# Kernel tuning notes

Hardware: AMD Instinct MI355X
Metric: run time of the kernel (lower is better)

## Reference

```python
import jax, jax.numpy as jnp
import numpy as np

NUM_EXPERTS = 8
IN_FEATURES = 2048
OUT_FEATURES = 5632
GROUP_SIZE = 64
NUM_TOKENS = 4096


def setup_inputs() -> dict:
    key = jax.random.key(0)
    k1, k2, k3, k4 = jax.random.split(key, 4)
    inp = jax.random.normal(k1, (NUM_TOKENS, IN_FEATURES), dtype=jnp.float32)
    # tokens are pre-sorted contiguously per expert; balanced routing
    tokens_per_expert = jnp.full((NUM_EXPERTS,), NUM_TOKENS // NUM_EXPERTS, dtype=jnp.int32)
    # int4 quantized weights stored as integer codes in [0, 16)
    weights = jax.random.randint(k2, (NUM_EXPERTS, IN_FEATURES, OUT_FEATURES), 0, 16, dtype=jnp.int32)
    n_groups = IN_FEATURES // GROUP_SIZE
    scales = jax.random.uniform(k3, (NUM_EXPERTS, n_groups, OUT_FEATURES, 1), dtype=jnp.float32,
                                minval=0.005, maxval=0.02)
    zeros = jax.random.normal(k4, (NUM_EXPERTS, n_groups, OUT_FEATURES, 1), dtype=jnp.float32) * 0.01
    scales_and_zeros = jnp.concatenate([scales, zeros], axis=-1)  # [E, K//G, N, 2]
    return {"input": inp, "tokens_per_expert": tokens_per_expert,
            "weights": weights, "scales_and_zeros": scales_and_zeros}


def _dequant(weights, scales_and_zeros):
    # torchao int4 convention: w = (q - 8) * scale + zero, grouped along K
    E, K, N = weights.shape
    n_groups = scales_and_zeros.shape[1]
    g = K // n_groups
    q = weights.astype(jnp.float32).reshape(E, n_groups, g, N)
    s = scales_and_zeros[..., 0][:, :, None, :]  # [E, K//G, 1, N]
    z = scales_and_zeros[..., 1][:, :, None, :]
    return ((q - 8.0) * s + z).reshape(E, K, N)


def reference(input, tokens_per_expert, weights, scales_and_zeros):
    num_tokens, K = input.shape
    E = weights.shape[0]
    W = _dequant(weights, scales_and_zeros)  # [E, K, N] float32
    # expert id of each (contiguous-sorted) token from cumsum boundaries
    cum = jnp.cumsum(tokens_per_expert)                      # [E]
    seg = jnp.searchsorted(cum, jnp.arange(num_tokens), side='right')  # [T]
    start = jnp.concatenate([jnp.zeros((1,), cum.dtype), cum[:-1]])
    pos = jnp.arange(num_tokens) - start[seg]                # slot within expert block
    # capacity-based grouped GEMM (balanced routing in setup: C = T // E)
    C = num_tokens // E
    buf = jnp.zeros((E, C, K), input.dtype).at[seg, pos].set(input)
    y = jnp.einsum('eck,ekn->ecn', buf, W)                   # per-expert GEMM
    return y[seg, pos]                                       # [T, N]
```

## Files before the change

### kernel.cpp

```cpp
#include <hip/hip_runtime.h>

#define NE    8
#define KDIM  2048
#define NDIM  5632
#define NTOK  4096
#define CAP   512
#define NGRP  32
#define BM    128
#define BN    128
#define BK    32
#define MT    4
#define NT    44
#define LDSS  40

typedef __attribute__((ext_vector_type(8))) short bf16x8;
typedef __attribute__((ext_vector_type(4))) short bf16x4;
typedef __attribute__((ext_vector_type(4))) float f32x4;

static __device__ __forceinline__ short f2bf(float f) {
    union { float f; unsigned u; } x; x.f = f;
    unsigned r = (x.u + 0x7fffu + ((x.u >> 16) & 1u)) >> 16;
    return (short)r;
}

__global__ __launch_bounds__(256, 2)
void hqq_gemm_kernel(const float* __restrict__ inp,
                     const int*   __restrict__ wq,
                     const float* __restrict__ sz,
                     float*       __restrict__ out)
{
    const int bid = blockIdx.x;
    const int e   = bid / (MT * NT);
    const int rem = bid % (MT * NT);
    const int nt  = rem >> 2;
    const int mt  = rem & 3;

    __shared__ __align__(16) short Alds[BM * LDSS];
    __shared__ __align__(16) short Blds[BN * LDSS];

    const int tid = threadIdx.x;
    const int m0  = e * CAP + mt * BM;
    const int n0  = nt * BN;

    const int a_kq  = tid & 7;
    const int a_row = tid >> 3;
    const int b_n   = tid & 127;
    const int b_h   = tid >> 7;

    const float* Ab  = inp + (size_t)m0 * KDIM;
    const int*   Wb  = wq  + (size_t)e * KDIM * NDIM + n0 + b_n;
    const float* SZb = sz  + (size_t)e * NGRP * (NDIM * 2) + (size_t)(n0 + b_n) * 2;

    f32x4 acc[4][4];
    #pragma unroll
    for (int i = 0; i < 4; ++i)
        #pragma unroll
        for (int j = 0; j < 4; ++j)
            acc[i][j] = (f32x4){0.f, 0.f, 0.f, 0.f};

    const int wave = tid >> 6;
    const int lane = tid & 63;
    const int wm = (wave >> 1) << 6;
    const int wn = (wave & 1) << 6;
    const int lr = lane & 15;
    const int lq = lane >> 4;

    for (int k0 = 0; k0 < KDIM; k0 += BK) {
        const int g = k0 >> 6;

        #pragma unroll
        for (int p = 0; p < 4; ++p) {
            const int row = a_row + p * 32;
            const float4 v = *(const float4*)(Ab + (size_t)row * KDIM + k0 + a_kq * 4);
            bf16x4 h;
            h[0] = f2bf(v.x); h[1] = f2bf(v.y); h[2] = f2bf(v.z); h[3] = f2bf(v.w);
            *(bf16x4*)&Alds[row * LDSS + a_kq * 4] = h;
        }

        const float2 s2 = *(const float2*)(SZb + (size_t)g * (NDIM * 2));
        const float s  = s2.x;
        const float z8 = s2.y - 8.f * s2.x;
        #pragma unroll
        for (int oo = 0; oo < 2; ++oo) {
            const int ko = b_h * 8 + oo * 16;
            const int* wp = Wb + (size_t)(k0 + ko) * NDIM;
            bf16x8 bb;
            #pragma unroll
            for (int j = 0; j < 8; ++j) {
                const float q = (float)wp[(size_t)j * NDIM];
                bb[j] = f2bf(fmaf(q, s, z8));
            }
            *(bf16x8*)&Blds[b_n * LDSS + ko] = bb;
        }

        __syncthreads();

        bf16x8 af[4], bfv[4];
        #pragma unroll
        for (int i = 0; i < 4; ++i)
            af[i] = *(const bf16x8*)&Alds[(wm + i * 16 + lr) * LDSS + lq * 8];
        #pragma unroll
        for (int j = 0; j < 4; ++j)
            bfv[j] = *(const bf16x8*)&Blds[(wn + j * 16 + lr) * LDSS + lq * 8];
        #pragma unroll
        for (int i = 0; i < 4; ++i)
            #pragma unroll
            for (int j = 0; j < 4; ++j)
                acc[i][j] = __builtin_amdgcn_mfma_f32_16x16x32_bf16(af[i], bfv[j], acc[i][j], 0, 0, 0);

        __syncthreads();
    }

    const int orow0 = m0 + wm + lq * 4;
    const int ocol0 = n0 + wn + lr;
    #pragma unroll
    for (int i = 0; i < 4; ++i)
        #pragma unroll
        for (int r = 0; r < 4; ++r) {
            float* op = out + (size_t)(orow0 + i * 16 + r) * NDIM + ocol0;
            #pragma unroll
            for (int j = 0; j < 4; ++j)
                op[j * 16] = acc[i][j][r];
        }
}

extern "C" void kernel_launch(void* const* d_in, const int* in_sizes, int n_in,
                              void* d_out, int out_size, void* d_ws, size_t ws_size,
                              hipStream_t stream) {
    const float* inp = (const float*)d_in[0];
    const int*   wq  = (const int*)d_in[2];
    const float* sz  = (const float*)d_in[3];
    float*       out = (float*)d_out;

    dim3 grid(NE * MT * NT);
    hqq_gemm_kernel<<<grid, dim3(256), 0, stream>>>(inp, wq, sz, out);
}
```

Baseline: 683.5 us.

## Prepack int4 weights into nibbles and pre-convert activations to bf16

A new pre-pass kernel packs the int32 weight codes into 4-bit nibbles (eight per word) and converts the fp32 input to bf16 in workspace memory. The GEMM then reads the packed weights and bf16 activations, which reduces the bytes the four M-tiles pull per expert and drops the per-tile conversions. The pre-pass still reads all int32 weights once and adds a launch. The original kernel is kept as a fallback when the workspace is too small.

```diff
diff --git a/kernel.cpp b/kernel.cpp
--- a/kernel.cpp
+++ b/kernel.cpp
@@ -13,6 +13,13 @@
 #define NT    44
 #define LDSS  40
 
+#define K8      (KDIM / 8)
+#define NBLK_N  (NDIM / 256)
+#define PACK_BLOCKS (NE * K8 * NBLK_N)
+#define ACV_BLOCKS  (NTOK * KDIM / (8 * 256))
+#define PACKED_BYTES ((size_t)NE * K8 * NDIM * 4)
+#define ABF_BYTES    ((size_t)NTOK * KDIM * 2)
+
 typedef __attribute__((ext_vector_type(8))) short bf16x8;
 typedef __attribute__((ext_vector_type(4))) short bf16x4;
 typedef __attribute__((ext_vector_type(4))) float f32x4;
@@ -23,11 +30,39 @@
     return (short)r;
 }
 
+__global__ __launch_bounds__(256)
+void pack_kernel(const int* __restrict__ wq, const float* __restrict__ inp,
+                 unsigned* __restrict__ pw, unsigned short* __restrict__ abf)
+{
+    const int bid = blockIdx.x;
+    if (bid < PACK_BLOCKS) {
+        const int e  = bid / (K8 * NBLK_N);
+        const int r  = bid % (K8 * NBLK_N);
+        const int k8 = r / NBLK_N;
+        const int nb = r % NBLK_N;
+        const int n  = nb * 256 + threadIdx.x;
+        const int* src = wq + ((size_t)e * KDIM + k8 * 8) * NDIM + n;
+        unsigned v = 0;
+        #pragma unroll
+        for (int j = 0; j < 8; ++j)
+            v |= (unsigned)(src[(size_t)j * NDIM] & 15) << (4 * j);
+        pw[((size_t)e * K8 + k8) * NDIM + n] = v;
+    } else {
+        const size_t t = (size_t)(bid - PACK_BLOCKS) * 256 + threadIdx.x;
+        const float4* p = (const float4*)inp + t * 2;
+        const float4 v0 = p[0], v1 = p[1];
+        bf16x8 h;
+        h[0] = f2bf(v0.x); h[1] = f2bf(v0.y); h[2] = f2bf(v0.z); h[3] = f2bf(v0.w);
+        h[4] = f2bf(v1.x); h[5] = f2bf(v1.y); h[6] = f2bf(v1.z); h[7] = f2bf(v1.w);
+        *((bf16x8*)abf + t) = h;
+    }
+}
+
 __global__ __launch_bounds__(256, 2)
-void hqq_gemm_kernel(const float* __restrict__ inp,
-                     const int*   __restrict__ wq,
-                     const float* __restrict__ sz,
-                     float*       __restrict__ out)
+void hqq_gemm2(const unsigned short* __restrict__ abf,
+               const unsigned*       __restrict__ pw,
+               const float*          __restrict__ sz,
+               float*                __restrict__ out)
 {
     const int bid = blockIdx.x;
     const int e   = bid / (MT * NT);
@@ -42,14 +77,14 @@
     const int m0  = e * CAP + mt * BM;
     const int n0  = nt * BN;
 
-    const int a_kq  = tid & 7;
-    const int a_row = tid >> 3;
+    const int a_kq  = tid & 3;
+    const int a_row = tid >> 2;
     const int b_n   = tid & 127;
     const int b_h   = tid >> 7;
 
-    const float* Ab  = inp + (size_t)m0 * KDIM;
-    const int*   Wb  = wq  + (size_t)e * KDIM * NDIM + n0 + b_n;
-    const float* SZb = sz  + (size_t)e * NGRP * (NDIM * 2) + (size_t)(n0 + b_n) * 2;
+    const unsigned short* Ab = abf + (size_t)m0 * KDIM;
+    const unsigned*       Wb = pw  + (size_t)e * K8 * NDIM + n0 + b_n;
+    const float*          SZb = sz + (size_t)e * NGRP * (NDIM * 2) + (size_t)(n0 + b_n) * 2;
 
     f32x4 acc[4][4];
     #pragma unroll
@@ -69,6 +104,103 @@
         const int g = k0 >> 6;
 
         #pragma unroll
+        for (int p = 0; p < 2; ++p) {
+            const int row = a_row + p * 64;
+            const bf16x8 v = *(const bf16x8*)(Ab + (size_t)row * KDIM + k0 + a_kq * 8);
+            *(bf16x8*)&Alds[row * LDSS + a_kq * 8] = v;
+        }
+
+        const float2 s2 = *(const float2*)(SZb + (size_t)g * (NDIM * 2));
+        const float s  = s2.x;
+        const float z8 = s2.y - 8.f * s2.x;
+        const unsigned* wp = Wb + ((size_t)(k0 >> 3) + b_h * 2) * NDIM;
+        const unsigned u0 = wp[0];
+        const unsigned u1 = wp[NDIM];
+        bf16x8 bb0, bb1;
+        #pragma unroll
+        for (int j = 0; j < 8; ++j) {
+            bb0[j] = f2bf(fmaf((float)((u0 >> (4 * j)) & 15u), s, z8));
+            bb1[j] = f2bf(fmaf((float)((u1 >> (4 * j)) & 15u), s, z8));
+        }
+        *(bf16x8*)&Blds[b_n * LDSS + b_h * 16]     = bb0;
+        *(bf16x8*)&Blds[b_n * LDSS + b_h * 16 + 8] = bb1;
+
+        __syncthreads();
+
+        bf16x8 af[4], bfv[4];
+        #pragma unroll
+        for (int i = 0; i < 4; ++i)
+            af[i] = *(const bf16x8*)&Alds[(wm + i * 16 + lr) * LDSS + lq * 8];
+        #pragma unroll
+        for (int j = 0; j < 4; ++j)
+            bfv[j] = *(const bf16x8*)&Blds[(wn + j * 16 + lr) * LDSS + lq * 8];
+        #pragma unroll
+        for (int i = 0; i < 4; ++i)
+            #pragma unroll
+            for (int j = 0; j < 4; ++j)
+                acc[i][j] = __builtin_amdgcn_mfma_f32_16x16x32_bf16(af[i], bfv[j], acc[i][j], 0, 0, 0);
+
+        __syncthreads();
+    }
+
+    const int orow0 = m0 + wm + lq * 4;
+    const int ocol0 = n0 + wn + lr;
+    #pragma unroll
+    for (int i = 0; i < 4; ++i)
+        #pragma unroll
+        for (int r = 0; r < 4; ++r) {
+            float* op = out + (size_t)(orow0 + i * 16 + r) * NDIM + ocol0;
+            #pragma unroll
+            for (int j = 0; j < 4; ++j)
+                op[j * 16] = acc[i][j][r];
+        }
+}
+
+__global__ __launch_bounds__(256, 2)
+void hqq_gemm_fallback(const float* __restrict__ inp,
+                       const int*   __restrict__ wq,
+                       const float* __restrict__ sz,
+                       float*       __restrict__ out)
+{
+    const int bid = blockIdx.x;
+    const int e   = bid / (MT * NT);
+    const int rem = bid % (MT * NT);
+    const int nt  = rem >> 2;
+    const int mt  = rem & 3;
+
+    __shared__ __align__(16) short Alds[BM * LDSS];
+    __shared__ __align__(16) short Blds[BN * LDSS];
+
+    const int tid = threadIdx.x;
+    const int m0  = e * CAP + mt * BM;
+    const int n0  = nt * BN;
+
+    const int a_kq  = tid & 7;
+    const int a_row = tid >> 3;
+    const int b_n   = tid & 127;
+    const int b_h   = tid >> 7;
+
+    const float* Ab  = inp + (size_t)m0 * KDIM;
+    const int*   Wb  = wq  + (size_t)e * KDIM * NDIM + n0 + b_n;
+    const float* SZb = sz  + (size_t)e * NGRP * (NDIM * 2) + (size_t)(n0 + b_n) * 2;
+
+    f32x4 acc[4][4];
+    #pragma unroll
+    for (int i = 0; i < 4; ++i)
+        #pragma unroll
+        for (int j = 0; j < 4; ++j)
+            acc[i][j] = (f32x4){0.f, 0.f, 0.f, 0.f};
+
+    const int wave = tid >> 6;
+    const int lane = tid & 63;
+    const int wm = (wave >> 1) << 6;
+    const int wn = (wave & 1) << 6;
+    const int lr = lane & 15;
+    const int lq = lane >> 4;
+
+    for (int k0 = 0; k0 < KDIM; k0 += BK) {
+        const int g = k0 >> 6;
+        #pragma unroll
         for (int p = 0; p < 4; ++p) {
             const int row = a_row + p * 32;
             const float4 v = *(const float4*)(Ab + (size_t)row * KDIM + k0 + a_kq * 4);
@@ -76,7 +208,6 @@
             h[0] = f2bf(v.x); h[1] = f2bf(v.y); h[2] = f2bf(v.z); h[3] = f2bf(v.w);
             *(bf16x4*)&Alds[row * LDSS + a_kq * 4] = h;
         }
-
         const float2 s2 = *(const float2*)(SZb + (size_t)g * (NDIM * 2));
         const float s  = s2.x;
         const float z8 = s2.y - 8.f * s2.x;
@@ -92,9 +223,7 @@
             }
             *(bf16x8*)&Blds[b_n * LDSS + ko] = bb;
         }
-
-        __syncthreads();
-
+        __syncthreads();
         bf16x8 af[4], bfv[4];
         #pragma unroll
         for (int i = 0; i < 4; ++i)
@@ -107,7 +236,6 @@
             #pragma unroll
             for (int j = 0; j < 4; ++j)
                 acc[i][j] = __builtin_amdgcn_mfma_f32_16x16x32_bf16(af[i], bfv[j], acc[i][j], 0, 0, 0);
-
         __syncthreads();
     }
 
@@ -132,6 +260,12 @@
     const float* sz  = (const float*)d_in[3];
     float*       out = (float*)d_out;
 
-    dim3 grid(NE * MT * NT);
-    hqq_gemm_kernel<<<grid, dim3(256), 0, stream>>>(inp, wq, sz, out);
-}
+    if (ws_size >= PACKED_BYTES + ABF_BYTES) {
+        unsigned*       pw  = (unsigned*)d_ws;
+        unsigned short* abf = (unsigned short*)((char*)d_ws + PACKED_BYTES);
+        pack_kernel<<<dim3(PACK_BLOCKS + ACV_BLOCKS), dim3(256), 0, stream>>>(wq, inp, pw, abf);
+        hqq_gemm2<<<dim3(NE * MT * NT), dim3(256), 0, stream>>>(abf, pw, sz, out);
+    } else {
+        hqq_gemm_fallback<<<dim3(NE * MT * NT), dim3(256), 0, stream>>>(inp, wq, sz, out);
+    }
+}
```

Measured after the change: 674.1 us. No clear change (-1.4%).
